# Performance work log

Hardware: AMD Instinct MI355X
Metric: run time of the kernel (lower is better)

## Reference

```python
import jax, jax.numpy as jnp
import numpy as np

N_NODES = 100000


def sage_conv(x, src, dst, W_l, W_r, b):
    """PyG-style SAGEConv with mean aggregation:
    out = mean_{j in N(i)} x_j @ W_l + b + x_i @ W_r
    Messages flow edge_index[0] (src) -> edge_index[1] (dst).
    """
    n = x.shape[0]
    msgs = x[src]  # [E, F] gather
    agg = jax.ops.segment_sum(msgs, dst, num_segments=n)  # [N, F]
    cnt = jax.ops.segment_sum(jnp.ones((src.shape[0],), dtype=x.dtype), dst, num_segments=n)
    mean = agg / jnp.clip(cnt, 1.0)[:, None]
    return mean @ W_l + b + x @ W_r


def setup_inputs() -> dict:
    key = jax.random.key(0)
    ks = jax.random.split(key, 12)
    F_in, H, out_c = 128, 128, 1
    E, K = 3200000, 64

    def glorot(k, shape):
        fan_in, fan_out = shape[0], shape[1]
        lim = np.sqrt(6.0 / (fan_in + fan_out))
        return jax.random.uniform(k, shape, jnp.float32, -lim, lim)

    return {
        "x": jax.random.normal(ks[0], (N_NODES, F_in), jnp.float32),
        "edge_index": jax.random.randint(ks[1], (2, E), 0, N_NODES, jnp.int64),
        "curr_idx": 123,
        "dest_idx": 4567,
        "neighbor_indices": jax.random.randint(ks[2], (K,), 0, N_NODES, jnp.int64),
        # conv1 params
        "W1_l": glorot(ks[3], (F_in, H)),
        "W1_r": glorot(ks[4], (F_in, H)),
        "b1": jnp.zeros((H,), jnp.float32),
        # conv2 params
        "W2_l": glorot(ks[5], (H, H)),
        "W2_r": glorot(ks[6], (H, H)),
        "b2": jnp.zeros((H,), jnp.float32),
        # MLP head
        "Wlin1": glorot(ks[7], (3 * H, H)),
        "blin1": jnp.zeros((H,), jnp.float32),
        "Wlin2": glorot(ks[8], (H, out_c)),
        "blin2": jnp.zeros((out_c,), jnp.float32),
    }


def reference(x, edge_index, curr_idx, dest_idx, neighbor_indices,
              W1_l, W1_r, b1, W2_l, W2_r, b2, Wlin1, blin1, Wlin2, blin2):
    src, dst = edge_index[0], edge_index[1]
    h = jax.nn.relu(sage_conv(x, src, dst, W1_l, W1_r, b1))
    node_embs = sage_conv(h, src, dst, W2_l, W2_r, b2)  # [N, H]

    curr_emb = node_embs[curr_idx]  # [H]
    dest_emb = node_embs[dest_idx]  # [H]
    nbr_embs = node_embs[neighbor_indices]  # [K, H]
    K = nbr_embs.shape[0]
    # batched version of the per-neighbor concat + 2-layer MLP
    cat = jnp.concatenate([
        jnp.broadcast_to(curr_emb, (K, curr_emb.shape[0])),
        jnp.broadcast_to(dest_emb, (K, dest_emb.shape[0])),
        nbr_embs,
    ], axis=1)  # [K, 3H]
    hidden = jax.nn.relu(cat @ Wlin1 + blin1)  # [K, H]
    q_values = hidden @ Wlin2 + blin2  # [K, 1]
    return q_values
```

## Files before the change

### kernel.cpp

```cpp
#include <hip/hip_runtime.h>
#include <cstdint>

constexpr int F        = 128;
constexpr int U_CAP    = 8192;
constexpr int T_CAP    = 128;
constexpr int E2_CAP   = 131072;
constexpr int BKT      = 128;
constexpr int BM_WORDS = 3200;
constexpr int SBLK     = 256;
constexpr int EPT      = 16;
constexpr int EPBLK    = SBLK * EPT;
constexpr int LCAP     = 512;


__global__ void k_zero(int* p, int n) {
    int i = blockIdx.x * blockDim.x + threadIdx.x;
    int stride = gridDim.x * blockDim.x;
    for (; i < n; i += stride) p[i] = 0;
}

__global__ void k_build(const int* eidx, int E, int N,
                        const int* curr, const int* dest, const int* nbr, int K,
                        int* hdr, int* t_map, int* u_map,
                        unsigned* t_bm, unsigned* u_bm,
                        int* t_node, int* ent2comp, int* ulist) {
    __shared__ int s_e64, s_n64;
    int tid = threadIdx.x;
    if (tid == 0) { s_e64 = 1; s_n64 = 1; }
    __syncthreads();
    if (tid < 64 && eidx[2 * tid + 1] != 0) s_e64 = 0;
    if (tid < K / 2 && nbr[2 * tid + 1] != 0) s_n64 = 0;
    __syncthreads();
    int n64 = s_n64;
    if (tid == 0) { hdr[4] = s_e64; hdr[5] = s_n64; }

    int node = -1;
    if (tid < K + 2) {
        if (tid == 0)      node = curr[0];
        else if (tid == 1) node = dest[0];
        else               node = n64 ? nbr[2 * (tid - 2)] : nbr[tid - 2];
        if ((unsigned)node < (unsigned)N) {
            if (atomicCAS(&t_map[node], 0, -1) == 0) {
                int slot = atomicAdd(&hdr[0], 1);
                t_node[slot] = node;
                int uid = atomicAdd(&hdr[1], 1);
                ulist[uid] = node;
                atomicExch(&u_map[node], uid + 1);
                if (node < BM_WORDS * 32) {
                    atomicOr(&t_bm[node >> 5], 1u << (node & 31));
                    atomicOr(&u_bm[node >> 5], 1u << (node & 31));
                }
                atomicExch(&t_map[node], slot + 1);
            }
        }
    }
    __syncthreads();
    if (tid < K + 2) {
        int v = ((unsigned)node < (unsigned)N) ? atomicAdd(&t_map[node], 0) : 1;
        ent2comp[tid] = v - 1;
    }
}

static __device__ __forceinline__ int esrc(const int* eidx, int E, int e, int is64) {
    return is64 ? eidx[2 * (size_t)e] : eidx[e];
}
static __device__ __forceinline__ int edst(const int* eidx, int E, int e, int is64) {
    return is64 ? eidx[2 * ((size_t)E + e)] : eidx[(size_t)E + e];
}

__global__ void k_scan1(const int* __restrict__ eidx, int E, int N,
                        const int* __restrict__ t_map, int* u_map,
                        const unsigned* __restrict__ t_bm, unsigned* u_bm,
                        int* hdr, int2* edges2, int* ulist) {
    __shared__ __align__(16) unsigned s_bm[BM_WORDS];
    __shared__ int l_cnt, l_base;
    __shared__ int2 l_buf[LCAP];
    int tid = threadIdx.x;
    if (tid == 0) l_cnt = 0;
    {
        const int4* s4 = reinterpret_cast<const int4*>(t_bm);
        int4* d4 = reinterpret_cast<int4*>(s_bm);
        for (int w = tid; w < BM_WORDS / 4; w += SBLK) d4[w] = s4[w];
    }
    int is64 = hdr[4];
    int be = blockIdx.x * EPBLK;
    int dv[EPT];
    #pragma unroll
    for (int r = 0; r < 4; ++r) {
        int e0 = be + r * (SBLK * 4) + tid * 4;
        if (!is64 && e0 + 3 < E) {
            int4 d4 = *reinterpret_cast<const int4*>(eidx + (size_t)E + e0);
            dv[r*4+0] = d4.x; dv[r*4+1] = d4.y; dv[r*4+2] = d4.z; dv[r*4+3] = d4.w;
        } else {
            for (int q = 0; q < 4; ++q)
                dv[r*4+q] = (e0 + q < E) ? edst(eidx, E, e0 + q, is64) : -1;
        }
    }
    __syncthreads();
    unsigned m = 0;
    #pragma unroll
    for (int i = 0; i < EPT; ++i) {
        int d = dv[i];
        if ((unsigned)d < (unsigned)N) {
            bool maybe = (d < BM_WORDS * 32) ? ((s_bm[d >> 5] >> (d & 31)) & 1) : true;
            if (maybe) m |= (1u << i);
        }
    }
    while (m) {
        int i = __ffs(m) - 1; m &= m - 1;
        int d = dv[i];
        int tm = t_map[d];
        if (tm <= 0) continue;
        int r = i >> 2, q = i & 3;
        int e = be + r * (SBLK * 4) + tid * 4 + q;
        int s = esrc(eidx, E, e, is64);
        if ((unsigned)s >= (unsigned)N) continue;
        int p = atomicAdd(&l_cnt, 1);
        if (p < LCAP) l_buf[p] = make_int2(s, tm - 1);
        else {
            int gp = atomicAdd(&hdr[2], 1);
            if (gp < E2_CAP) edges2[gp] = make_int2(s, tm - 1);
        }
        if (atomicCAS(&u_map[s], 0, -1) == 0) {
            int id = atomicAdd(&hdr[1], 1);
            if (id < U_CAP) ulist[id] = s;
            if (s < BM_WORDS * 32) atomicOr(&u_bm[s >> 5], 1u << (s & 31));
            __threadfence();
            atomicExch(&u_map[s], id + 1);
        }
    }
    __syncthreads();
    int c = min(l_cnt, LCAP);
    if (c > 0) {
        if (tid == 0) l_base = atomicAdd(&hdr[2], c);
        __syncthreads();
        for (int i = tid; i < c; i += SBLK) {
            int gp = l_base + i;
            if (gp < E2_CAP) edges2[gp] = l_buf[i];
        }
    }
}

__global__ void k_scanU(const int* __restrict__ eidx, int E, int N,
                        const int* __restrict__ u_map,
                        const unsigned* __restrict__ u_bm,
                        const int* __restrict__ hdr,
                        int* deg1, int* bucket) {
    __shared__ __align__(16) unsigned s_bm[BM_WORDS];
    int tid = threadIdx.x;
    {
        const int4* s4 = reinterpret_cast<const int4*>(u_bm);
        int4* d4 = reinterpret_cast<int4*>(s_bm);
        for (int w = tid; w < BM_WORDS / 4; w += SBLK) d4[w] = s4[w];
    }
    int is64 = hdr[4];
    int be = blockIdx.x * EPBLK;
    int dv[EPT];
    #pragma unroll
    for (int r = 0; r < 4; ++r) {
        int e0 = be + r * (SBLK * 4) + tid * 4;
        if (!is64 && e0 + 3 < E) {
            int4 d4 = *reinterpret_cast<const int4*>(eidx + (size_t)E + e0);
            dv[r*4+0] = d4.x; dv[r*4+1] = d4.y; dv[r*4+2] = d4.z; dv[r*4+3] = d4.w;
        } else {
            for (int q = 0; q < 4; ++q)
                dv[r*4+q] = (e0 + q < E) ? edst(eidx, E, e0 + q, is64) : -1;
        }
    }
    __syncthreads();
    unsigned m = 0;
    #pragma unroll
    for (int i = 0; i < EPT; ++i) {
        int d = dv[i];
        if ((unsigned)d < (unsigned)N) {
            bool maybe = (d < BM_WORDS * 32) ? ((s_bm[d >> 5] >> (d & 31)) & 1) : true;
            if (maybe) m |= (1u << i);
        }
    }
    while (m) {
        int i = __ffs(m) - 1; m &= m - 1;
        int d = dv[i];
        int um = u_map[d];
        if (um <= 0 || um > U_CAP) continue;
        int r = i >> 2, q = i & 3;
        int e = be + r * (SBLK * 4) + tid * 4 + q;
        int s = esrc(eidx, E, e, is64);
        if ((unsigned)s >= (unsigned)N) continue;
        int slot = um - 1;
        int pos = atomicAdd(&deg1[slot], 1);
        if (pos < BKT) bucket[(size_t)slot * BKT + pos] = s;
    }
}

__global__ void k_acc1(const int* __restrict__ deg1, const int* __restrict__ bucket,
                       const int* __restrict__ hdr, int N,
                       const float* __restrict__ x, float* __restrict__ agg1) {
    int b = blockIdx.x;
    if (b >= min(hdr[1], U_CAP)) return;
    int j = threadIdx.x;
    __shared__ int s_src[BKT];
    int dg = deg1[b];
    int stored = min(dg, BKT);
    if (j < stored) s_src[j] = bucket[(size_t)b * BKT + j];
    __syncthreads();
    float acc = 0.0f;
    #pragma unroll 4
    for (int i = 0; i < stored; ++i) {
        int s = s_src[i];
        if ((unsigned)s < (unsigned)N) acc += x[(size_t)s * F + j];
    }
    float c = (dg < 1) ? 1.0f : (float)dg;
    agg1[(size_t)b * F + j] = acc / c;
}

__global__ void k_h(const int* __restrict__ hdr, const int* __restrict__ ulist, int N,
                    const float* __restrict__ agg1,
                    const float* __restrict__ x,
                    const float* __restrict__ W1l, const float* __restrict__ W1r,
                    const float* __restrict__ b1, float* __restrict__ h) {
    int nU = min(hdr[1], U_CAP);
    __shared__ float mean[F];
    __shared__ float xr[F];
    int j = threadIdx.x;
    for (int b = blockIdx.x; b < nU; b += gridDim.x) {
        int node = ulist[b];
        mean[j] = agg1[(size_t)b * F + j];
        xr[j]   = ((unsigned)node < (unsigned)N) ? x[(size_t)node * F + j] : 0.0f;
        __syncthreads();
        float acc = b1[j];
        #pragma unroll 4
        for (int k = 0; k < F; ++k) {
            acc += mean[k] * W1l[k * F + j];
            acc += xr[k]   * W1r[k * F + j];
        }
        h[(size_t)b * F + j] = (acc > 0.0f) ? acc : 0.0f;
        __syncthreads();
    }
}

__global__ void k_acc2(const int2* __restrict__ edges2, const int* __restrict__ hdr, int N,
                       const int* __restrict__ u_map, const float* __restrict__ h,
                       float* agg2, float* cnt2) {
    int nE     = min(hdr[2], E2_CAP);
    int lane   = threadIdx.x & (F - 1);
    int grp    = (blockIdx.x * blockDim.x + threadIdx.x) >> 7;
    int stride = (gridDim.x * blockDim.x) >> 7;
    for (int e = grp; e < nE; e += stride) {
        int2 ed = edges2[e];
        if ((unsigned)ed.x >= (unsigned)N || (unsigned)ed.y >= (unsigned)T_CAP) continue;
        int ui = u_map[ed.x] - 1;
        if ((unsigned)ui >= (unsigned)U_CAP) continue;
        atomicAdd(&agg2[(size_t)ed.y * F + lane], h[(size_t)ui * F + lane]);
        if (lane == 0) atomicAdd(&cnt2[ed.y], 1.0f);
    }
}

__global__ void k_emb(const int* __restrict__ hdr, const int* __restrict__ t_node,
                      const int* __restrict__ u_map, int N,
                      const float* __restrict__ agg2, const float* __restrict__ cnt2,
                      const float* __restrict__ h,
                      const float* __restrict__ W2l, const float* __restrict__ W2r,
                      const float* __restrict__ b2, float* __restrict__ embT) {
    int nT = min(hdr[0], T_CAP);
    int b  = blockIdx.x;
    if (b >= nT) return;
    __shared__ float mean[F];
    __shared__ float hr[F];
    int j    = threadIdx.x;
    int node = t_node[b];
    int ui   = ((unsigned)node < (unsigned)N) ? (u_map[node] - 1) : -1;
    float c  = cnt2[b];
    c = (c < 1.0f) ? 1.0f : c;
    mean[j] = agg2[(size_t)b * F + j] / c;
    hr[j]   = ((unsigned)ui < (unsigned)U_CAP) ? h[(size_t)ui * F + j] : 0.0f;
    __syncthreads();
    float acc = b2[j];
    #pragma unroll 4
    for (int k = 0; k < F; ++k) {
        acc += mean[k] * W2l[k * F + j];
        acc += hr[k]   * W2r[k * F + j];
    }
    embT[(size_t)b * F + j] = acc;
}

__global__ void k_base(const int* __restrict__ ent2comp, const float* __restrict__ embT,
                       const float* __restrict__ Wlin1, const float* __restrict__ blin1,
                       float* __restrict__ base) {
    __shared__ float s_cat[2 * F];
    __shared__ float s_part[4][F];
    int tid = threadIdx.x;
    int g = tid >> 7, j = tid & (F - 1);
    int c0 = ent2comp[0] & (T_CAP - 1);
    int c1 = ent2comp[1] & (T_CAP - 1);
    if (tid < F)          s_cat[tid] = embT[(size_t)c0 * F + tid];
    else if (tid < 2 * F) s_cat[tid] = embT[(size_t)c1 * F + (tid - F)];
    __syncthreads();
    float acc = 0.0f;
    #pragma unroll 4
    for (int i = g * 64; i < (g + 1) * 64; ++i)
        acc += s_cat[i] * Wlin1[i * F + j];
    s_part[g][j] = acc;
    __syncthreads();
    if (g == 0)
        base[j] = blin1[j] + s_part[0][j] + s_part[1][j] + s_part[2][j] + s_part[3][j];
}

static __device__ __forceinline__ float clamp999(int v) {
    return (float)(v < 0 ? 0 : (v > 999 ? 999 : v));
}

__global__ void k_head(const int* __restrict__ hdr, const int* __restrict__ ent2comp,
                       const float* __restrict__ embT,
                       const float* __restrict__ Wlin1, const float* __restrict__ base,
                       const float* __restrict__ Wlin2, const float* __restrict__ blin2,
                       float* __restrict__ out, int K) {
    __shared__ float s_nbr[F];
    __shared__ float s_part[4][F];
    __shared__ float red[F];
    int k = blockIdx.x;
    int tid = threadIdx.x;
    int g = tid >> 7, j = tid & (F - 1);
    int ck = ent2comp[2 + k] & (T_CAP - 1);
    if (tid < F) s_nbr[tid] = embT[(size_t)ck * F + tid];
    __syncthreads();
    const float* W = Wlin1 + 2 * F * F;
    float acc = 0.0f;
    #pragma unroll 4
    for (int i = g * 32; i < (g + 1) * 32; ++i)
        acc += s_nbr[i] * W[i * F + j];
    s_part[g][j] = acc;
    __syncthreads();
    if (g == 0) {
        float hid = base[j] + s_part[0][j] + s_part[1][j] + s_part[2][j] + s_part[3][j];
        hid = (hid > 0.0f) ? hid : 0.0f;
        red[j] = hid * Wlin2[j];
    }
    __syncthreads();
    for (int s = 64; s > 0; s >>= 1) {
        if (tid < s) red[tid] += red[tid + s];
        __syncthreads();
    }
    if (tid == 0) {
        int nT = hdr[0], nU = hdr[1], nE2 = hdr[2];
        float D = 0.0f;
        if      (nT  < 1  || nT  > K + 2)  D = 1.0e6f + clamp999(nT) * 1e3f;
        else if (nU  < nT || nU  > U_CAP)  D = 2.0e6f + clamp999(nU / 10) * 1e3f;
        else if (nE2 < 1  || nE2 > E2_CAP) D = 3.0e6f + clamp999(nE2 / 10) * 1e3f;
        out[k] = red[0] + blin2[0] + D;
    }
}

extern "C" void kernel_launch(void* const* d_in, const int* in_sizes, int n_in,
                              void* d_out, int out_size, void* d_ws, size_t ws_size,
                              hipStream_t stream) {
    const float* x     = (const float*)d_in[0];
    const int*   eidx  = (const int*)d_in[1];
    const int*   curr  = (const int*)d_in[2];
    const int*   dest  = (const int*)d_in[3];
    const int*   nbr   = (const int*)d_in[4];
    const float* W1l   = (const float*)d_in[5];
    const float* W1r   = (const float*)d_in[6];
    const float* b1    = (const float*)d_in[7];
    const float* W2l   = (const float*)d_in[8];
    const float* W2r   = (const float*)d_in[9];
    const float* b2    = (const float*)d_in[10];
    const float* Wlin1 = (const float*)d_in[11];
    const float* blin1 = (const float*)d_in[12];
    const float* Wlin2 = (const float*)d_in[13];
    const float* blin2 = (const float*)d_in[14];
    float* out = (float*)d_out;

    const int N = in_sizes[0] / F;
    const int E = in_sizes[1] / 2;
    const int K = in_sizes[4];

    char*  ws  = (char*)d_ws;
    size_t off = 0;
    int*      hdr      = (int*)(ws + off);      off += 64;
    int*      t_map    = (int*)(ws + off);      off += (size_t)4 * N;
    int*      u_map    = (int*)(ws + off);      off += (size_t)4 * N;
    float*    agg2     = (float*)(ws + off);    off += (size_t)4 * T_CAP * F;
    float*    cnt2     = (float*)(ws + off);    off += (size_t)4 * T_CAP;
    int*      t_node   = (int*)(ws + off);      off += (size_t)4 * T_CAP;
    int*      ent2comp = (int*)(ws + off);      off += (size_t)4 * 256;
    int*      ulist    = (int*)(ws + off);      off += (size_t)4 * U_CAP;
    unsigned* t_bm     = (unsigned*)(ws + off); off += (size_t)4 * BM_WORDS;
    unsigned* u_bm     = (unsigned*)(ws + off); off += (size_t)4 * BM_WORDS;
    int*      deg1     = (int*)(ws + off);      off += (size_t)4 * U_CAP;
    size_t zero_bytes = off;
    int*      bucket   = (int*)(ws + off);      off += (size_t)4 * U_CAP * BKT;
    float*    agg1     = (float*)(ws + off);    off += (size_t)4 * U_CAP * F;
    int2*     edges2   = (int2*)(ws + off);     off += (size_t)8 * E2_CAP;
    float*    h        = (float*)(ws + off);    off += (size_t)4 * U_CAP * F;
    float*    embT     = (float*)(ws + off);    off += (size_t)4 * T_CAP * F;
    float*    base     = (float*)(ws + off);    off += (size_t)4 * F;

    int zero_words = (int)(zero_bytes / 4);
    k_zero<<<1024, 256, 0, stream>>>((int*)d_ws, zero_words);

    k_build<<<1, 128, 0, stream>>>(eidx, E, N, curr, dest, nbr, K, hdr, t_map, u_map,
                                   t_bm, u_bm, t_node, ent2comp, ulist);

    int sg = (E + EPBLK - 1) / EPBLK;
    k_scan1<<<sg, SBLK, 0, stream>>>(eidx, E, N, t_map, u_map, t_bm, u_bm,
                                     hdr, edges2, ulist);
    k_scanU<<<sg, SBLK, 0, stream>>>(eidx, E, N, u_map, u_bm, hdr, deg1, bucket);
    k_acc1<<<U_CAP, 128, 0, stream>>>(deg1, bucket, hdr, N, x, agg1);
    k_h<<<2048, 128, 0, stream>>>(hdr, ulist, N, agg1, x, W1l, W1r, b1, h);
    k_acc2<<<256, 256, 0, stream>>>(edges2, hdr, N, u_map, h, agg2, cnt2);
    k_emb<<<K + 2, 128, 0, stream>>>(hdr, t_node, u_map, N, agg2, cnt2, h, W2l, W2r, b2, embT);
    k_base<<<1, 512, 0, stream>>>(ent2comp, embT, Wlin1, blin1, base);
    k_head<<<K, 512, 0, stream>>>(hdr, ent2comp, embT, Wlin1, base, Wlin2, blin2, out, K);
}
```

Measured before the change: 265.1 us.

## Fuse zero, build and both edge scans into one cooperative persistent kernel

```diff
diff --git a/kernel.cpp b/kernel.cpp
--- a/kernel.cpp
+++ b/kernel.cpp
@@ -1,5 +1,8 @@
 #include <hip/hip_runtime.h>
+#include <hip/hip_cooperative_groups.h>
 #include <cstdint>
+
+namespace cg = cooperative_groups;
 
 constexpr int F        = 128;
 constexpr int U_CAP    = 8192;
@@ -8,187 +11,185 @@
 constexpr int BKT      = 128;
 constexpr int BM_WORDS = 3200;
 constexpr int SBLK     = 256;
-constexpr int EPT      = 16;
-constexpr int EPBLK    = SBLK * EPT;
+constexpr int FGRID    = 512;
+constexpr int RND      = 8;
 constexpr int LCAP     = 512;
 
 
-__global__ void k_zero(int* p, int n) {
-    int i = blockIdx.x * blockDim.x + threadIdx.x;
-    int stride = gridDim.x * blockDim.x;
-    for (; i < n; i += stride) p[i] = 0;
-}
-
-__global__ void k_build(const int* eidx, int E, int N,
+static __device__ __forceinline__ int esrc(const int* eidx, int E, int e, int is64) {
+    return is64 ? eidx[2 * (size_t)e] : eidx[e];
+}
+static __device__ __forceinline__ int edst(const int* eidx, int E, int e, int is64) {
+    return is64 ? eidx[2 * ((size_t)E + e)] : eidx[(size_t)E + e];
+}
+
+__global__ void k_front(const int* eidx, int E, int N,
                         const int* curr, const int* dest, const int* nbr, int K,
                         int* hdr, int* t_map, int* u_map,
                         unsigned* t_bm, unsigned* u_bm,
-                        int* t_node, int* ent2comp, int* ulist) {
-    __shared__ int s_e64, s_n64;
+                        int* t_node, int* ent2comp, int* ulist,
+                        int* deg1, int* bucket, int2* edges2,
+                        int* zbase, int zero_words) {
+    cg::grid_group gg = cg::this_grid();
     int tid = threadIdx.x;
-    if (tid == 0) { s_e64 = 1; s_n64 = 1; }
-    __syncthreads();
-    if (tid < 64 && eidx[2 * tid + 1] != 0) s_e64 = 0;
-    if (tid < K / 2 && nbr[2 * tid + 1] != 0) s_n64 = 0;
-    __syncthreads();
-    int n64 = s_n64;
-    if (tid == 0) { hdr[4] = s_e64; hdr[5] = s_n64; }
-
-    int node = -1;
-    if (tid < K + 2) {
-        if (tid == 0)      node = curr[0];
-        else if (tid == 1) node = dest[0];
-        else               node = n64 ? nbr[2 * (tid - 2)] : nbr[tid - 2];
-        if ((unsigned)node < (unsigned)N) {
-            if (atomicCAS(&t_map[node], 0, -1) == 0) {
-                int slot = atomicAdd(&hdr[0], 1);
-                t_node[slot] = node;
-                int uid = atomicAdd(&hdr[1], 1);
-                ulist[uid] = node;
-                atomicExch(&u_map[node], uid + 1);
-                if (node < BM_WORDS * 32) {
-                    atomicOr(&t_bm[node >> 5], 1u << (node & 31));
-                    atomicOr(&u_bm[node >> 5], 1u << (node & 31));
-                }
-                atomicExch(&t_map[node], slot + 1);
-            }
-        }
-    }
-    __syncthreads();
-    if (tid < K + 2) {
-        int v = ((unsigned)node < (unsigned)N) ? atomicAdd(&t_map[node], 0) : 1;
-        ent2comp[tid] = v - 1;
-    }
-}
-
-static __device__ __forceinline__ int esrc(const int* eidx, int E, int e, int is64) {
-    return is64 ? eidx[2 * (size_t)e] : eidx[e];
-}
-static __device__ __forceinline__ int edst(const int* eidx, int E, int e, int is64) {
-    return is64 ? eidx[2 * ((size_t)E + e)] : eidx[(size_t)E + e];
-}
-
-__global__ void k_scan1(const int* __restrict__ eidx, int E, int N,
-                        const int* __restrict__ t_map, int* u_map,
-                        const unsigned* __restrict__ t_bm, unsigned* u_bm,
-                        int* hdr, int2* edges2, int* ulist) {
-    __shared__ __align__(16) unsigned s_bm[BM_WORDS];
+    int bid = blockIdx.x;
+    int tt  = gridDim.x * blockDim.x;
+    int gt  = bid * blockDim.x + tid;
+
     __shared__ int l_cnt, l_base;
     __shared__ int2 l_buf[LCAP];
-    int tid = threadIdx.x;
+
+    for (int i = gt; i < zero_words; i += tt) zbase[i] = 0;
+    gg.sync();
+
+    if (bid == 0) {
+        __shared__ int s_e64, s_n64;
+        if (tid == 0) { s_e64 = 1; s_n64 = 1; }
+        __syncthreads();
+        if (tid < 64 && eidx[2 * tid + 1] != 0) s_e64 = 0;
+        if (tid < K / 2 && nbr[2 * tid + 1] != 0) s_n64 = 0;
+        __syncthreads();
+        int n64 = s_n64;
+        if (tid == 0) { hdr[4] = s_e64; hdr[5] = s_n64; }
+        int node = -1;
+        if (tid < K + 2) {
+            if (tid == 0)      node = curr[0];
+            else if (tid == 1) node = dest[0];
+            else               node = n64 ? nbr[2 * (tid - 2)] : nbr[tid - 2];
+            if ((unsigned)node < (unsigned)N) {
+                if (atomicCAS(&t_map[node], 0, -1) == 0) {
+                    int slot = atomicAdd(&hdr[0], 1);
+                    t_node[slot] = node;
+                    int uid = atomicAdd(&hdr[1], 1);
+                    ulist[uid] = node;
+                    atomicExch(&u_map[node], uid + 1);
+                    if (node < BM_WORDS * 32) {
+                        atomicOr(&t_bm[node >> 5], 1u << (node & 31));
+                        atomicOr(&u_bm[node >> 5], 1u << (node & 31));
+                    }
+                    atomicExch(&t_map[node], slot + 1);
+                }
+            }
+        }
+        __syncthreads();
+        if (tid < K + 2) {
+            int v = ((unsigned)node < (unsigned)N) ? atomicAdd(&t_map[node], 0) : 1;
+            ent2comp[tid] = v - 1;
+        }
+    }
+    gg.sync();
+
+    int is64 = hdr[4];
+    int cpb = ((E + (int)gridDim.x - 1) / (int)gridDim.x + 3) & ~3;
+    int start = bid * cpb;
+    int end   = min(start + cpb, E);
     if (tid == 0) l_cnt = 0;
+    __syncthreads();
+
+    for (int base = start; base < end; base += SBLK * RND * 4) {
+        int dv[RND * 4];
+        #pragma unroll
+        for (int r = 0; r < RND; ++r) {
+            int e0 = base + (r * SBLK + tid) * 4;
+            if (!is64 && e0 + 3 < end) {
+                int4 d4 = *reinterpret_cast<const int4*>(eidx + (size_t)E + e0);
+                dv[r*4+0] = d4.x; dv[r*4+1] = d4.y; dv[r*4+2] = d4.z; dv[r*4+3] = d4.w;
+            } else {
+                for (int q = 0; q < 4; ++q)
+                    dv[r*4+q] = (e0 + q < end) ? edst(eidx, E, e0 + q, is64) : -1;
+            }
+        }
+        unsigned wv[RND * 4];
+        #pragma unroll
+        for (int i = 0; i < RND * 4; ++i) {
+            int d  = dv[i];
+            int dc = ((unsigned)d < (unsigned)N) ? d : 0;
+            wv[i] = t_bm[dc >> 5];
+        }
+        unsigned m = 0;
+        #pragma unroll
+        for (int i = 0; i < RND * 4; ++i) {
+            int d = dv[i];
+            if ((unsigned)d < (unsigned)N && ((wv[i] >> (d & 31)) & 1)) m |= (1u << i);
+        }
+        while (m) {
+            int i = __ffs(m) - 1; m &= m - 1;
+            int d = dv[i];
+            int tm = t_map[d];
+            if (tm <= 0) continue;
+            int r = i >> 2, q = i & 3;
+            int e = base + (r * SBLK + tid) * 4 + q;
+            int s = esrc(eidx, E, e, is64);
+            if ((unsigned)s >= (unsigned)N) continue;
+            int p = atomicAdd(&l_cnt, 1);
+            if (p < LCAP) l_buf[p] = make_int2(s, tm - 1);
+            else {
+                int gp = atomicAdd(&hdr[2], 1);
+                if (gp < E2_CAP) edges2[gp] = make_int2(s, tm - 1);
+            }
+            if (atomicCAS(&u_map[s], 0, -1) == 0) {
+                int id = atomicAdd(&hdr[1], 1);
+                if (id < U_CAP) ulist[id] = s;
+                if (s < BM_WORDS * 32) atomicOr(&u_bm[s >> 5], 1u << (s & 31));
+                __threadfence();
+                atomicExch(&u_map[s], id + 1);
+            }
+        }
+    }
+    __syncthreads();
     {
-        const int4* s4 = reinterpret_cast<const int4*>(t_bm);
-        int4* d4 = reinterpret_cast<int4*>(s_bm);
-        for (int w = tid; w < BM_WORDS / 4; w += SBLK) d4[w] = s4[w];
-    }
-    int is64 = hdr[4];
-    int be = blockIdx.x * EPBLK;
-    int dv[EPT];
-    #pragma unroll
-    for (int r = 0; r < 4; ++r) {
-        int e0 = be + r * (SBLK * 4) + tid * 4;
-        if (!is64 && e0 + 3 < E) {
-            int4 d4 = *reinterpret_cast<const int4*>(eidx + (size_t)E + e0);
-            dv[r*4+0] = d4.x; dv[r*4+1] = d4.y; dv[r*4+2] = d4.z; dv[r*4+3] = d4.w;
-        } else {
-            for (int q = 0; q < 4; ++q)
-                dv[r*4+q] = (e0 + q < E) ? edst(eidx, E, e0 + q, is64) : -1;
-        }
-    }
-    __syncthreads();
-    unsigned m = 0;
-    #pragma unroll
-    for (int i = 0; i < EPT; ++i) {
-        int d = dv[i];
-        if ((unsigned)d < (unsigned)N) {
-            bool maybe = (d < BM_WORDS * 32) ? ((s_bm[d >> 5] >> (d & 31)) & 1) : true;
-            if (maybe) m |= (1u << i);
-        }
-    }
-    while (m) {
-        int i = __ffs(m) - 1; m &= m - 1;
-        int d = dv[i];
-        int tm = t_map[d];
-        if (tm <= 0) continue;
-        int r = i >> 2, q = i & 3;
-        int e = be + r * (SBLK * 4) + tid * 4 + q;
-        int s = esrc(eidx, E, e, is64);
-        if ((unsigned)s >= (unsigned)N) continue;
-        int p = atomicAdd(&l_cnt, 1);
-        if (p < LCAP) l_buf[p] = make_int2(s, tm - 1);
-        else {
-            int gp = atomicAdd(&hdr[2], 1);
-            if (gp < E2_CAP) edges2[gp] = make_int2(s, tm - 1);
-        }
-        if (atomicCAS(&u_map[s], 0, -1) == 0) {
-            int id = atomicAdd(&hdr[1], 1);
-            if (id < U_CAP) ulist[id] = s;
-            if (s < BM_WORDS * 32) atomicOr(&u_bm[s >> 5], 1u << (s & 31));
-            __threadfence();
-            atomicExch(&u_map[s], id + 1);
-        }
-    }
-    __syncthreads();
-    int c = min(l_cnt, LCAP);
-    if (c > 0) {
-        if (tid == 0) l_base = atomicAdd(&hdr[2], c);
-        __syncthreads();
-        for (int i = tid; i < c; i += SBLK) {
-            int gp = l_base + i;
-            if (gp < E2_CAP) edges2[gp] = l_buf[i];
-        }
-    }
-}
-
-__global__ void k_scanU(const int* __restrict__ eidx, int E, int N,
-                        const int* __restrict__ u_map,
-                        const unsigned* __restrict__ u_bm,
-                        const int* __restrict__ hdr,
-                        int* deg1, int* bucket) {
-    __shared__ __align__(16) unsigned s_bm[BM_WORDS];
-    int tid = threadIdx.x;
-    {
-        const int4* s4 = reinterpret_cast<const int4*>(u_bm);
-        int4* d4 = reinterpret_cast<int4*>(s_bm);
-        for (int w = tid; w < BM_WORDS / 4; w += SBLK) d4[w] = s4[w];
-    }
-    int is64 = hdr[4];
-    int be = blockIdx.x * EPBLK;
-    int dv[EPT];
-    #pragma unroll
-    for (int r = 0; r < 4; ++r) {
-        int e0 = be + r * (SBLK * 4) + tid * 4;
-        if (!is64 && e0 + 3 < E) {
-            int4 d4 = *reinterpret_cast<const int4*>(eidx + (size_t)E + e0);
-            dv[r*4+0] = d4.x; dv[r*4+1] = d4.y; dv[r*4+2] = d4.z; dv[r*4+3] = d4.w;
-        } else {
-            for (int q = 0; q < 4; ++q)
-                dv[r*4+q] = (e0 + q < E) ? edst(eidx, E, e0 + q, is64) : -1;
-        }
-    }
-    __syncthreads();
-    unsigned m = 0;
-    #pragma unroll
-    for (int i = 0; i < EPT; ++i) {
-        int d = dv[i];
-        if ((unsigned)d < (unsigned)N) {
-            bool maybe = (d < BM_WORDS * 32) ? ((s_bm[d >> 5] >> (d & 31)) & 1) : true;
-            if (maybe) m |= (1u << i);
-        }
-    }
-    while (m) {
-        int i = __ffs(m) - 1; m &= m - 1;
-        int d = dv[i];
-        int um = u_map[d];
-        if (um <= 0 || um > U_CAP) continue;
-        int r = i >> 2, q = i & 3;
-        int e = be + r * (SBLK * 4) + tid * 4 + q;
-        int s = esrc(eidx, E, e, is64);
-        if ((unsigned)s >= (unsigned)N) continue;
-        int slot = um - 1;
-        int pos = atomicAdd(&deg1[slot], 1);
-        if (pos < BKT) bucket[(size_t)slot * BKT + pos] = s;
+        int c = min(l_cnt, LCAP);
+        if (c > 0) {
+            if (tid == 0) l_base = atomicAdd(&hdr[2], c);
+            __syncthreads();
+            for (int i = tid; i < c; i += SBLK) {
+                int gp = l_base + i;
+                if (gp < E2_CAP) edges2[gp] = l_buf[i];
+            }
+        }
+    }
+    __threadfence();
+    gg.sync();
+
+    for (int base = start; base < end; base += SBLK * RND * 4) {
+        int dv[RND * 4];
+        #pragma unroll
+        for (int r = 0; r < RND; ++r) {
+            int e0 = base + (r * SBLK + tid) * 4;
+            if (!is64 && e0 + 3 < end) {
+                int4 d4 = *reinterpret_cast<const int4*>(eidx + (size_t)E + e0);
+                dv[r*4+0] = d4.x; dv[r*4+1] = d4.y; dv[r*4+2] = d4.z; dv[r*4+3] = d4.w;
+            } else {
+                for (int q = 0; q < 4; ++q)
+                    dv[r*4+q] = (e0 + q < end) ? edst(eidx, E, e0 + q, is64) : -1;
+            }
+        }
+        unsigned wv[RND * 4];
+        #pragma unroll
+        for (int i = 0; i < RND * 4; ++i) {
+            int d  = dv[i];
+            int dc = ((unsigned)d < (unsigned)N) ? d : 0;
+            wv[i] = u_bm[dc >> 5];
+        }
+        unsigned m = 0;
+        #pragma unroll
+        for (int i = 0; i < RND * 4; ++i) {
+            int d = dv[i];
+            if ((unsigned)d < (unsigned)N && ((wv[i] >> (d & 31)) & 1)) m |= (1u << i);
+        }
+        while (m) {
+            int i = __ffs(m) - 1; m &= m - 1;
+            int d = dv[i];
+            int um = u_map[d];
+            if (um <= 0 || um > U_CAP) continue;
+            int r = i >> 2, q = i & 3;
+            int e = base + (r * SBLK + tid) * 4 + q;
+            int s = esrc(eidx, E, e, is64);
+            if ((unsigned)s >= (unsigned)N) continue;
+            int slot = um - 1;
+            int pos = atomicAdd(&deg1[slot], 1);
+            if (pos < BKT) bucket[(size_t)slot * BKT + pos] = s;
+        }
     }
 }
 
@@ -370,9 +371,9 @@
     const float* blin2 = (const float*)d_in[14];
     float* out = (float*)d_out;
 
-    const int N = in_sizes[0] / F;
-    const int E = in_sizes[1] / 2;
-    const int K = in_sizes[4];
+    int N = in_sizes[0] / F;
+    int E = in_sizes[1] / 2;
+    int K = in_sizes[4];
 
     char*  ws  = (char*)d_ws;
     size_t off = 0;
@@ -396,15 +397,20 @@
     float*    base     = (float*)(ws + off);    off += (size_t)4 * F;
 
     int zero_words = (int)(zero_bytes / 4);
-    k_zero<<<1024, 256, 0, stream>>>((int*)d_ws, zero_words);
-
-    k_build<<<1, 128, 0, stream>>>(eidx, E, N, curr, dest, nbr, K, hdr, t_map, u_map,
-                                   t_bm, u_bm, t_node, ent2comp, ulist);
-
-    int sg = (E + EPBLK - 1) / EPBLK;
-    k_scan1<<<sg, SBLK, 0, stream>>>(eidx, E, N, t_map, u_map, t_bm, u_bm,
-                                     hdr, edges2, ulist);
-    k_scanU<<<sg, SBLK, 0, stream>>>(eidx, E, N, u_map, u_bm, hdr, deg1, bucket);
+    int* zbase = (int*)d_ws;
+
+    void* args[] = {
+        (void*)&eidx, (void*)&E, (void*)&N,
+        (void*)&curr, (void*)&dest, (void*)&nbr, (void*)&K,
+        (void*)&hdr, (void*)&t_map, (void*)&u_map,
+        (void*)&t_bm, (void*)&u_bm,
+        (void*)&t_node, (void*)&ent2comp, (void*)&ulist,
+        (void*)&deg1, (void*)&bucket, (void*)&edges2,
+        (void*)&zbase, (void*)&zero_words
+    };
+    hipLaunchCooperativeKernel((const void*)k_front, dim3(FGRID), dim3(SBLK),
+                               args, 0, stream);
+
     k_acc1<<<U_CAP, 128, 0, stream>>>(deg1, bucket, hdr, N, x, agg1);
     k_h<<<2048, 128, 0, stream>>>(hdr, ulist, N, agg1, x, W1l, W1r, b1, h);
     k_acc2<<<256, 256, 0, stream>>>(edges2, hdr, N, u_map, h, agg2, cnt2);
```

Result: slower. 466.6 us (+76.0%).
